# Kernel optimization log

Hardware: AMD Instinct MI355X
Metric: run time of the kernel (lower is better)

Reference implementation:

```python
import jax, jax.numpy as jnp
import numpy as np

N = 1048576   # total points across batch
C = 64        # in_planes
B = 16        # number of ragged segments (point clouds)
EPS = 1e-5


def setup_inputs() -> dict:
    key = jax.random.key(0)
    ks = jax.random.split(key, 4)
    x = jax.random.normal(ks[0], (N, C), dtype=jnp.float32)
    # cumulative end-offsets, strictly increasing, last == N
    rng = np.random.default_rng(0)
    w = rng.random(B) + 0.5
    ends = np.round(np.cumsum(w) / w.sum() * N).astype(np.int64)
    ends[-1] = N
    o = jnp.asarray(ends)
    # linear2: Linear(C, C) + ReLU (applied to per-segment mean)
    W2 = jax.random.normal(ks[1], (C, C), dtype=jnp.float32) / np.float32(np.sqrt(C))
    b2 = jnp.zeros((C,), jnp.float32)
    # linear1: BasicMLP(2C -> C): Linear + norm + ReLU
    W1 = jax.random.normal(ks[2], (2 * C, C), dtype=jnp.float32) / np.float32(np.sqrt(2 * C))
    b1 = jnp.zeros((C,), jnp.float32)
    gamma = jnp.ones((C,), jnp.float32)
    beta = jnp.zeros((C,), jnp.float32)
    return dict(x=x, o=o, W2=W2, b2=b2, W1=W1, b1=b1, gamma=gamma, beta=beta)


def reference(x, o, W2, b2, W1, b1, gamma, beta):
    n = x.shape[0]
    nseg = o.shape[0]
    # segment id of each point from cumulative offsets o
    seg = jnp.searchsorted(o, jnp.arange(n), side='right')          # [N]
    counts = jnp.diff(o, prepend=0).astype(x.dtype)                 # [B]
    # per-segment mean pool (x_b.sum(0) / cnt)
    sums = jax.ops.segment_sum(x, seg, num_segments=nseg)           # [B, C]
    means = sums / counts[:, None]
    # linear2: Linear + ReLU on the pooled vector
    xb = jax.nn.relu(means @ W2 + b2)                               # [B, C]
    # broadcast-repeat pooled feature back to points, concat with x
    h = jnp.concatenate([x, xb[seg]], axis=1)                       # [N, 2C]
    # linear1: Linear -> norm (LayerNorm stand-in for conditional norm) -> ReLU
    h = h @ W1 + b1                                                 # [N, C]
    mu = jnp.mean(h, axis=-1, keepdims=True)
    var = jnp.var(h, axis=-1, keepdims=True)
    h = (h - mu) * jax.lax.rsqrt(var + EPS) * gamma + beta
    return jax.nn.relu(h)
```

## Files before the change

### kernel.cpp

```cpp
#include <hip/hip_runtime.h>
#include <hip/hip_bf16.h>
#include <cstddef>

constexpr int C = 64;
constexpr int B = 16;

typedef __attribute__((ext_vector_type(8))) short bf16x8;
typedef __attribute__((ext_vector_type(4))) float f32x4;
typedef __attribute__((ext_vector_type(4))) unsigned int u32x4;

__device__ inline unsigned short f2bf(float f) {
    unsigned u = __builtin_bit_cast(unsigned, f);
    unsigned r = (u + 0x7FFFu + ((u >> 16) & 1u)) >> 16;
    return (unsigned short)r;
}

__device__ inline unsigned pk2(float a, float b) {
    __hip_bfloat162 t = __float22bfloat162_rn(float2{a, b});
    unsigned u;
    __builtin_memcpy(&u, &t, 4);
    return u;
}

__device__ inline bf16x8 cvt8(float4 u, float4 v) {
    u32x4 r;
    r[0] = pk2(u.x, u.y);
    r[1] = pk2(u.z, u.w);
    r[2] = pk2(v.x, v.y);
    r[3] = pk2(v.z, v.w);
    return __builtin_bit_cast(bf16x8, r);
}

__global__ __launch_bounds__(256) void seg_sum_kernel(
    const float* __restrict__ x, const int* __restrict__ o,
    float* __restrict__ sums, int N, int rows_per_block)
{
    __shared__ float lsum[B * C];
    const int tid = threadIdx.x;
    for (int i = tid; i < B * C; i += 256) lsum[i] = 0.0f;
    __syncthreads();

    const int c4 = (tid & 15) * 4;
    const int r0 = tid >> 4;
    const int row_begin = blockIdx.x * rows_per_block;
    const int row_end   = min(N, row_begin + rows_per_block);

    float ax = 0.f, ay = 0.f, az = 0.f, aw = 0.f;
    int seg = 0;
    int endcur = o[0];

    for (int r = row_begin + r0; r < row_end; r += 16) {
        while (r >= endcur) {
            if (ax != 0.f || ay != 0.f || az != 0.f || aw != 0.f) {
                atomicAdd(&lsum[seg * C + c4 + 0], ax);
                atomicAdd(&lsum[seg * C + c4 + 1], ay);
                atomicAdd(&lsum[seg * C + c4 + 2], az);
                atomicAdd(&lsum[seg * C + c4 + 3], aw);
                ax = ay = az = aw = 0.f;
            }
            ++seg;
            endcur = o[seg];
        }
        const float4 v = *reinterpret_cast<const float4*>(x + (size_t)r * C + c4);
        ax += v.x; ay += v.y; az += v.z; aw += v.w;
    }
    if (ax != 0.f || ay != 0.f || az != 0.f || aw != 0.f) {
        atomicAdd(&lsum[seg * C + c4 + 0], ax);
        atomicAdd(&lsum[seg * C + c4 + 1], ay);
        atomicAdd(&lsum[seg * C + c4 + 2], az);
        atomicAdd(&lsum[seg * C + c4 + 3], aw);
    }
    __syncthreads();

    for (int i = tid; i < B * C; i += 256) {
        const float v = lsum[i];
        if (v != 0.f) atomicAdd(&sums[i], v);
    }
}

__global__ __launch_bounds__(256) void main_mfma_kernel(
    const float* __restrict__ x, const int* __restrict__ o,
    const float* __restrict__ sums,
    const float* __restrict__ W2, const float* __restrict__ b2,
    const float* __restrict__ W1, const float* __restrict__ b1,
    const float* __restrict__ gamma, const float* __restrict__ beta,
    float* __restrict__ out, int N, int rows_per_wave, int ngw)
{
    __shared__ float ms[B * C];
    __shared__ float xbs[B * C];
    __shared__ float vl[B * C];
    __shared__ unsigned short wbfs[4096];
    __shared__ int osh[B];

    const int tid = threadIdx.x;
    if (tid < B) osh[tid] = o[tid];
    __syncthreads();

    const int j = tid & 63;
    const int bq = tid >> 6;

#pragma unroll
    for (int q = 0; q < 4; ++q) {
        const int b = bq * 4 + q;
        const int cnt = osh[b] - (b ? osh[b - 1] : 0);
        ms[b * C + j] = sums[b * C + j] / (float)cnt;
    }
    __syncthreads();

    {
        float acc[4];
        const float bj = b2[j];
#pragma unroll
        for (int q = 0; q < 4; ++q) acc[q] = bj;
        for (int c = 0; c < C; ++c) {
            const float wv = W2[c * C + j];
#pragma unroll
            for (int q = 0; q < 4; ++q)
                acc[q] = fmaf(ms[(bq * 4 + q) * C + c], wv, acc[q]);
        }
#pragma unroll
        for (int q = 0; q < 4; ++q) xbs[(bq * 4 + q) * C + j] = fmaxf(acc[q], 0.f);
    }
    __syncthreads();

    {
        float acc[4];
        const float bj = b1[j];
#pragma unroll
        for (int q = 0; q < 4; ++q) acc[q] = bj;
        for (int jj = 0; jj < C; ++jj) {
            const float wv = W1[(C + jj) * C + j];
#pragma unroll
            for (int q = 0; q < 4; ++q)
                acc[q] = fmaf(xbs[(bq * 4 + q) * C + jj], wv, acc[q]);
        }
#pragma unroll
        for (int q = 0; q < 4; ++q) vl[(bq * 4 + q) * C + j] = acc[q];
    }

    for (int idx = tid; idx < 4096; idx += 256) {
        const int jj2 = idx & 7;
        const int ln  = (idx >> 3) & 63;
        const int tt  = (idx >> 9) & 1;
        const int ct  = idx >> 10;
        const int k   = tt * 32 + ((ln >> 4) * 8) + jj2;
        const int ch  = 4 * (ln & 15) + ct;
        wbfs[idx] = f2bf(W1[k * C + ch]);
    }
    __syncthreads();

    const int lane = tid & 63;
    const int wid  = tid >> 6;
    const int chb  = lane & 15;
    const int prow = (lane >> 4) * 4;

    bf16x8 wf[4][2];
#pragma unroll
    for (int ct = 0; ct < 4; ++ct)
#pragma unroll
        for (int t = 0; t < 2; ++t)
            wf[ct][t] = *reinterpret_cast<const bf16x8*>(wbfs + ((ct * 2 + t) * 64 + lane) * 8);

    const float4 g4  = *reinterpret_cast<const float4*>(gamma + 4 * chb);
    const float4 bt4 = *reinterpret_cast<const float4*>(beta  + 4 * chb);

    const int gw0 = blockIdx.x * 4 + wid;
    if (gw0 >= ngw) return;
    const int gw = ngw - 1 - gw0;
    const int p_begin = gw * rows_per_wave;
    if (p_begin >= N) return;
    const int p_end = min(N, p_begin + rows_per_wave);

    int seg = 0;
    while (p_begin >= osh[seg]) ++seg;
    float4 vb = *reinterpret_cast<const float4*>(vl + seg * C + 4 * chb);

    for (int p0 = p_begin; p0 < p_end; p0 += 16) {
        const float* xr = x + (size_t)(p0 + chb) * C + ((lane >> 4) * 8);
        const float4 a0 = *reinterpret_cast<const float4*>(xr);
        const float4 a1 = *reinterpret_cast<const float4*>(xr + 4);
        const float4 a2 = *reinterpret_cast<const float4*>(xr + 32);
        const float4 a3 = *reinterpret_cast<const float4*>(xr + 36);
        const bf16x8 A0 = cvt8(a0, a1);
        const bf16x8 A1 = cvt8(a2, a3);

        f32x4 acc[4];
#pragma unroll
        for (int ct = 0; ct < 4; ++ct) {
            acc[ct] = f32x4{0.f, 0.f, 0.f, 0.f};
            acc[ct] = __builtin_amdgcn_mfma_f32_16x16x32_bf16(A0, wf[ct][0], acc[ct], 0, 0, 0);
            acc[ct] = __builtin_amdgcn_mfma_f32_16x16x32_bf16(A1, wf[ct][1], acc[ct], 0, 0, 0);
        }

        float h[4][4];
        if (p0 + 16 <= osh[seg]) {
#pragma unroll
            for (int r = 0; r < 4; ++r) {
                h[0][r] = acc[0][r] + vb.x;
                h[1][r] = acc[1][r] + vb.y;
                h[2][r] = acc[2][r] + vb.z;
                h[3][r] = acc[3][r] + vb.w;
            }
        } else {
#pragma unroll
            for (int r = 0; r < 4; ++r) {
                const int p = p0 + prow + r;
                int s = seg;
                while (p >= osh[s]) ++s;
                const float4 vbs = *reinterpret_cast<const float4*>(vl + s * C + 4 * chb);
                h[0][r] = acc[0][r] + vbs.x;
                h[1][r] = acc[1][r] + vbs.y;
                h[2][r] = acc[2][r] + vbs.z;
                h[3][r] = acc[3][r] + vbs.w;
            }
        }

#pragma unroll
        for (int r = 0; r < 4; ++r) {
            float s_ = (h[0][r] + h[1][r]) + (h[2][r] + h[3][r]);
            float q_ = fmaf(h[0][r], h[0][r],
                       fmaf(h[1][r], h[1][r],
                       fmaf(h[2][r], h[2][r], h[3][r] * h[3][r])));
#pragma unroll
            for (int m = 1; m < 16; m <<= 1) {
                s_ += __shfl_xor(s_, m, 64);
                q_ += __shfl_xor(q_, m, 64);
            }
            const float mean = s_ * (1.0f / 64.0f);
            const float var  = q_ * (1.0f / 64.0f) - mean * mean;
            const float rs   = rsqrtf(var + 1e-5f);
            const int p = p0 + prow + r;

            f32x4 y;
            y[0] = fmaxf((h[0][r] - mean) * rs * g4.x + bt4.x, 0.f);
            y[1] = fmaxf((h[1][r] - mean) * rs * g4.y + bt4.y, 0.f);
            y[2] = fmaxf((h[2][r] - mean) * rs * g4.z + bt4.z, 0.f);
            y[3] = fmaxf((h[3][r] - mean) * rs * g4.w + bt4.w, 0.f);
            __builtin_nontemporal_store(y, reinterpret_cast<f32x4*>(out + (size_t)p * C + 4 * chb));
        }

        const int pn = p0 + 16;
        if (pn < p_end && pn >= osh[seg]) {
            while (pn >= osh[seg]) ++seg;
            vb = *reinterpret_cast<const float4*>(vl + seg * C + 4 * chb);
        }
    }
}

extern "C" void kernel_launch(void* const* d_in, const int* in_sizes, int n_in,
                              void* d_out, int out_size, void* d_ws, size_t ws_size,
                              hipStream_t stream) {
    const float* x     = (const float*)d_in[0];
    const int*   o     = (const int*)d_in[1];
    const float* W2    = (const float*)d_in[2];
    const float* b2    = (const float*)d_in[3];
    const float* W1    = (const float*)d_in[4];
    const float* b1    = (const float*)d_in[5];
    const float* gamma = (const float*)d_in[6];
    const float* beta  = (const float*)d_in[7];
    float* out = (float*)d_out;

    const int N = in_sizes[0] / C;

    float* sums = (float*)d_ws;

    (void)hipMemsetAsync(sums, 0, B * C * sizeof(float), stream);

    const int rpb = 512;
    const int gridA = (N + rpb - 1) / rpb;
    seg_sum_kernel<<<gridA, 256, 0, stream>>>(x, o, sums, N, rpb);

    const int rpw = 128;
    const int ngw = (N + rpw - 1) / rpw;
    const int gridC = (ngw + 3) / 4;
    main_mfma_kernel<<<gridC, 256, 0, stream>>>(x, o, sums, W2, b2, W1, b1,
                                                gamma, beta, out, N, rpw, ngw);
}
```

Before: 152.9 us.

## Software-prefetch next x tile in main kernel and widen seg-sum loads

The main MFMA kernel now loads the next 16-row tile of x into registers before running the current tile's MFMAs, so global memory latency overlaps compute. The segment-sum kernel has each thread accumulate 8 channels with two float4 loads, halving per-thread row stride overhead. The reversed wave ordering in the main kernel is removed, so waves walk forward through memory. The prefetch raises register pressure and may cost occupancy.

```diff
diff --git a/kernel.cpp b/kernel.cpp
--- a/kernel.cpp
+++ b/kernel.cpp
@@ -40,36 +40,33 @@
     for (int i = tid; i < B * C; i += 256) lsum[i] = 0.0f;
     __syncthreads();
 
-    const int c4 = (tid & 15) * 4;
-    const int r0 = tid >> 4;
+    const int c8 = (tid & 7) * 8;
+    const int r0 = tid >> 3;
     const int row_begin = blockIdx.x * rows_per_block;
     const int row_end   = min(N, row_begin + rows_per_block);
 
-    float ax = 0.f, ay = 0.f, az = 0.f, aw = 0.f;
+    float a[8];
+#pragma unroll
+    for (int i = 0; i < 8; ++i) a[i] = 0.f;
     int seg = 0;
     int endcur = o[0];
 
-    for (int r = row_begin + r0; r < row_end; r += 16) {
+    for (int r = row_begin + r0; r < row_end; r += 32) {
         while (r >= endcur) {
-            if (ax != 0.f || ay != 0.f || az != 0.f || aw != 0.f) {
-                atomicAdd(&lsum[seg * C + c4 + 0], ax);
-                atomicAdd(&lsum[seg * C + c4 + 1], ay);
-                atomicAdd(&lsum[seg * C + c4 + 2], az);
-                atomicAdd(&lsum[seg * C + c4 + 3], aw);
-                ax = ay = az = aw = 0.f;
-            }
+#pragma unroll
+            for (int i = 0; i < 8; ++i)
+                if (a[i] != 0.f) { atomicAdd(&lsum[seg * C + c8 + i], a[i]); a[i] = 0.f; }
             ++seg;
             endcur = o[seg];
         }
-        const float4 v = *reinterpret_cast<const float4*>(x + (size_t)r * C + c4);
-        ax += v.x; ay += v.y; az += v.z; aw += v.w;
-    }
-    if (ax != 0.f || ay != 0.f || az != 0.f || aw != 0.f) {
-        atomicAdd(&lsum[seg * C + c4 + 0], ax);
-        atomicAdd(&lsum[seg * C + c4 + 1], ay);
-        atomicAdd(&lsum[seg * C + c4 + 2], az);
-        atomicAdd(&lsum[seg * C + c4 + 3], aw);
-    }
+        const float4 v0 = *reinterpret_cast<const float4*>(x + (size_t)r * C + c8);
+        const float4 v1 = *reinterpret_cast<const float4*>(x + (size_t)r * C + c8 + 4);
+        a[0] += v0.x; a[1] += v0.y; a[2] += v0.z; a[3] += v0.w;
+        a[4] += v1.x; a[5] += v1.y; a[6] += v1.z; a[7] += v1.w;
+    }
+#pragma unroll
+    for (int i = 0; i < 8; ++i)
+        if (a[i] != 0.f) atomicAdd(&lsum[seg * C + c8 + i], a[i]);
     __syncthreads();
 
     for (int i = tid; i < B * C; i += 256) {
@@ -164,9 +161,8 @@
     const float4 g4  = *reinterpret_cast<const float4*>(gamma + 4 * chb);
     const float4 bt4 = *reinterpret_cast<const float4*>(beta  + 4 * chb);
 
-    const int gw0 = blockIdx.x * 4 + wid;
-    if (gw0 >= ngw) return;
-    const int gw = ngw - 1 - gw0;
+    const int gw = blockIdx.x * 4 + wid;
+    if (gw >= ngw) return;
     const int p_begin = gw * rows_per_wave;
     if (p_begin >= N) return;
     const int p_end = min(N, p_begin + rows_per_wave);
@@ -175,14 +171,24 @@
     while (p_begin >= osh[seg]) ++seg;
     float4 vb = *reinterpret_cast<const float4*>(vl + seg * C + 4 * chb);
 
+    const size_t lane_off = (size_t)chb * C + ((lane >> 4) * 8);
+    const float* xr = x + (size_t)p_begin * C + lane_off;
+    float4 a0 = *reinterpret_cast<const float4*>(xr);
+    float4 a1 = *reinterpret_cast<const float4*>(xr + 4);
+    float4 a2 = *reinterpret_cast<const float4*>(xr + 32);
+    float4 a3 = *reinterpret_cast<const float4*>(xr + 36);
+
     for (int p0 = p_begin; p0 < p_end; p0 += 16) {
-        const float* xr = x + (size_t)(p0 + chb) * C + ((lane >> 4) * 8);
-        const float4 a0 = *reinterpret_cast<const float4*>(xr);
-        const float4 a1 = *reinterpret_cast<const float4*>(xr + 4);
-        const float4 a2 = *reinterpret_cast<const float4*>(xr + 32);
-        const float4 a3 = *reinterpret_cast<const float4*>(xr + 36);
         const bf16x8 A0 = cvt8(a0, a1);
         const bf16x8 A1 = cvt8(a2, a3);
+
+        if (p0 + 16 < p_end) {
+            const float* xn = x + (size_t)(p0 + 16) * C + lane_off;
+            a0 = *reinterpret_cast<const float4*>(xn);
+            a1 = *reinterpret_cast<const float4*>(xn + 4);
+            a2 = *reinterpret_cast<const float4*>(xn + 32);
+            a3 = *reinterpret_cast<const float4*>(xn + 36);
+        }
 
         f32x4 acc[4];
 #pragma unroll
```

Result: slower. 157.9 us (+3.3%).
